# Kernel tuning notes

Measured on AMD Instinct MI355X. Metric: run time of the kernel, lower is better.

Reference implementation:

```python
import jax, jax.numpy as jnp
import numpy as np

EPS = 1e-12  # tf.math.l2_normalize epsilon

def _l2n(x, axis):
    # faithful to K.l2_normalize: x / sqrt(max(sum(x^2), eps))
    return x / jnp.sqrt(jnp.maximum(jnp.sum(x * x, axis=axis, keepdims=True), EPS))

def setup_inputs() -> dict:
    key = jax.random.key(0)
    k1, k2, k3 = jax.random.split(key, 3)
    B, T, D, P = 32, 1024, 256, 20
    inp_a = jax.random.normal(k1, (B, T, D), dtype=jnp.float32)
    inp_b = jax.random.normal(k2, (B, T, D), dtype=jnp.float32)
    # 'uniform' keras initializer -> U(-0.05, 0.05)
    W = jax.random.uniform(k3, (P, D), dtype=jnp.float32, minval=-0.05, maxval=0.05)
    return {"inp_a": inp_a, "inp_b": inp_b, "W": W}

def reference(inp_a, inp_b, W):
    # inp_a, inp_b: (B, T, D); W: (P, D)
    oa = _l2n(inp_a, -1)
    ob = _l2n(inp_b, -1)
    # K.batch_dot(ob, oa, axes=[1,1]) -> (B, D, D), contract over seq
    alpha = jnp.einsum('btd,bte->bde', ob, oa)
    alpha = _l2n(alpha, 1)
    # K.batch_dot(ob, alpha, axes=[2,1]) -> (B, T, D)
    hmean = jnp.einsum('btd,bde->bte', ob, alpha)
    # Per perspective i the original computes the (T,T) batch_dot of
    # l2norm(hmean*W_i) and l2norm(inp_a*W_i), then masks with eye(T) and sums
    # -> the diagonal, i.e. per-token cosine similarity. Since both vectors are
    # scaled by the same W_i, cos = <a*h, W_i^2> / (||a*W_i|| * ||h*W_i||),
    # computed directly in linear cost for all perspectives at once.
    W2 = W * W  # (P, D)
    num = jnp.einsum('btd,pd->btp', inp_a * hmean, W2)
    sa = jnp.einsum('btd,pd->btp', inp_a * inp_a, W2)
    sh = jnp.einsum('btd,pd->btp', hmean * hmean, W2)
    persp = num / (jnp.sqrt(jnp.maximum(sa, EPS)) * jnp.sqrt(jnp.maximum(sh, EPS)))
    return (persp, persp)
```

## Files before the change

### kernel.cpp

```cpp
#include <hip/hip_runtime.h>
#include <math.h>

#define BB 32
#define TT 1024
#define DD 256
#define PP 20
constexpr float EPS = 1e-12f;

typedef __attribute__((ext_vector_type(8))) short bf16x8;
typedef __attribute__((ext_vector_type(4))) float f32x4;

static __device__ __forceinline__ unsigned short f2bf(float f) {
    union { float f; unsigned int u; } c; c.f = f;
    const unsigned int u = c.u;
    return (unsigned short)((u + 0x7FFFu + ((u >> 16) & 1u)) >> 16);
}

__global__ __launch_bounds__(256) void k_prep(const float* __restrict__ in,
                                              unsigned short* __restrict__ outT,
                                              unsigned short* __restrict__ outN) {
    __shared__ unsigned short Tls[DD][66];
    const int b = blockIdx.y;
    const int t0 = blockIdx.x * 64;
    const int wave = threadIdx.x >> 6;
    const int lane = threadIdx.x & 63;
    const float* src = in + (size_t)b * TT * DD;
    for (int pass = 0; pass < 16; ++pass) {
        const int tl = pass * 4 + wave;
        const int t = t0 + tl;
        const float4 v =
            *reinterpret_cast<const float4*>(&src[(size_t)t * DD + lane * 4]);
        float ss = v.x * v.x + v.y * v.y + v.z * v.z + v.w * v.w;
#pragma unroll
        for (int off = 32; off; off >>= 1) ss += __shfl_xor(ss, off);
        const float sc = 1.0f / sqrtf(fmaxf(ss, EPS));
        Tls[lane * 4 + 0][tl] = f2bf(v.x * sc);
        Tls[lane * 4 + 1][tl] = f2bf(v.y * sc);
        Tls[lane * 4 + 2][tl] = f2bf(v.z * sc);
        Tls[lane * 4 + 3][tl] = f2bf(v.w * sc);
        if (outN) {
            ushort4 r;
            r.x = f2bf(v.x); r.y = f2bf(v.y); r.z = f2bf(v.z); r.w = f2bf(v.w);
            *reinterpret_cast<ushort4*>(&outN[((size_t)b * TT + t) * DD + lane * 4]) = r;
        }
    }
    __syncthreads();
    const int d = threadIdx.x;
    unsigned short* dst = outT + ((size_t)b * DD + d) * TT + t0;
#pragma unroll
    for (int k = 0; k < 8; ++k) {
        unsigned short tmp[8];
#pragma unroll
        for (int j = 0; j < 8; ++j) tmp[j] = Tls[d][k * 8 + j];
        *reinterpret_cast<uint4*>(&dst[k * 8]) = *reinterpret_cast<const uint4*>(tmp);
    }
}

template <int M, int N, int K, int KS>
__global__ __launch_bounds__(256) void k_gemm(const unsigned short* __restrict__ A,
                                              const unsigned short* __restrict__ B,
                                              float* __restrict__ C) {
    __shared__ unsigned short As[2][64][40];
    __shared__ unsigned short Bs[2][64][40];
    const int tid = threadIdx.x;
    const int b = blockIdx.y;
    constexpr int NTILES = N / 64;
    constexpr int KSL = K / KS;
    const int m0 = (blockIdx.x / NTILES) * 64;
    const int n0 = (blockIdx.x % NTILES) * 64;
    const int kbeg = blockIdx.z * KSL;
    const unsigned short* pA = A + (size_t)b * M * K + (size_t)m0 * K + kbeg;
    const unsigned short* pB = B + (size_t)b * N * K + (size_t)n0 * K + kbeg;
    const int srow = tid >> 2;
    const int skoff = (tid & 3) * 8;
    const int wave = tid >> 6;
    const int lane = tid & 63;
    const int wm = (wave >> 1) * 32;
    const int wn = (wave & 1) * 32;
    const int fr = lane & 15;
    const int fc = lane >> 4;
    f32x4 acc[2][2] = {};
    uint4 ra, rb;

    ra = *reinterpret_cast<const uint4*>(&pA[(size_t)srow * K + skoff]);
    rb = *reinterpret_cast<const uint4*>(&pB[(size_t)srow * K + skoff]);
    *reinterpret_cast<uint4*>(&As[0][srow][skoff]) = ra;
    *reinterpret_cast<uint4*>(&Bs[0][srow][skoff]) = rb;

    constexpr int NT = KSL / 32;
    for (int t = 0; t < NT; ++t) {
        if (t + 1 < NT) {
            const int k0 = (t + 1) * 32;
            ra = *reinterpret_cast<const uint4*>(&pA[(size_t)srow * K + k0 + skoff]);
            rb = *reinterpret_cast<const uint4*>(&pB[(size_t)srow * K + k0 + skoff]);
        }
        __syncthreads();
        const int cur = t & 1;
        bf16x8 af[2], bfr[2];
#pragma unroll
        for (int i = 0; i < 2; ++i) {
            af[i]  = *reinterpret_cast<const bf16x8*>(&As[cur][wm + i * 16 + fr][fc * 8]);
            bfr[i] = *reinterpret_cast<const bf16x8*>(&Bs[cur][wn + i * 16 + fr][fc * 8]);
        }
#pragma unroll
        for (int i = 0; i < 2; ++i)
#pragma unroll
            for (int j = 0; j < 2; ++j)
                acc[i][j] = __builtin_amdgcn_mfma_f32_16x16x32_bf16(af[i], bfr[j],
                                                                    acc[i][j], 0, 0, 0);
        if (t + 1 < NT) {
            const int nxt = (t + 1) & 1;
            *reinterpret_cast<uint4*>(&As[nxt][srow][skoff]) = ra;
            *reinterpret_cast<uint4*>(&Bs[nxt][srow][skoff]) = rb;
        }
    }
    float* pC = C + (size_t)blockIdx.z * BB * M * N + (size_t)b * M * N;
#pragma unroll
    for (int i = 0; i < 2; ++i)
#pragma unroll
        for (int j = 0; j < 2; ++j) {
            const int rbase = m0 + wm + i * 16 + fc * 4;
            const int col = n0 + wn + j * 16 + fr;
#pragma unroll
            for (int r = 0; r < 4; ++r)
                pC[(size_t)(rbase + r) * N + col] = acc[i][j][r];
        }
}

__global__ __launch_bounds__(256) void k_alphanorm2(const float* __restrict__ p0,
                                                    const float* __restrict__ p1,
                                                    unsigned short* __restrict__ dst) {
    const int wave = threadIdx.x >> 6;
    const int lane = threadIdx.x & 63;
    const size_t row = (size_t)blockIdx.x * 4 + wave;
    float4 v = reinterpret_cast<const float4*>(p0 + row * DD)[lane];
    if (p1) {
        const float4 w = reinterpret_cast<const float4*>(p1 + row * DD)[lane];
        v.x += w.x; v.y += w.y; v.z += w.z; v.w += w.w;
    }
    float s = v.x * v.x + v.y * v.y + v.z * v.z + v.w * v.w;
#pragma unroll
    for (int off = 32; off; off >>= 1) s += __shfl_xor(s, off);
    const float sc = 1.0f / sqrtf(fmaxf(s, EPS));
    ushort4 r;
    r.x = f2bf(v.x * sc); r.y = f2bf(v.y * sc);
    r.z = f2bf(v.z * sc); r.w = f2bf(v.w * sc);
    reinterpret_cast<ushort4*>(dst + row * DD)[lane] = r;
}

__global__ __launch_bounds__(256) void k_persp2(const float* __restrict__ inp_a,
                                                const float* __restrict__ hmean,
                                                const float* __restrict__ W,
                                                float* __restrict__ out) {
    __shared__ uint4 Bpk[8 * 2 * 64];
    const int tid = threadIdx.x;
#pragma unroll
    for (int i = 0; i < 4; ++i) {
        const int ne = tid + i * 256;
        const int kstep = ne >> 7;
        const int j = (ne >> 6) & 1;
        const int ln = ne & 63;
        const int p = j * 16 + (ln & 15);
        const int k0 = kstep * 32 + (ln >> 4) * 8;
        unsigned short w8[8];
        if (p < PP) {
#pragma unroll
            for (int e = 0; e < 8; ++e) {
                const float w = W[p * DD + k0 + e];
                w8[e] = f2bf(w * w);
            }
        } else {
#pragma unroll
            for (int e = 0; e < 8; ++e) w8[e] = 0;
        }
        Bpk[ne] = *reinterpret_cast<const uint4*>(w8);
    }
    __syncthreads();

    const int wave = tid >> 6;
    const int lane = tid & 63;
    const int fr = lane & 15;
    const int fc = lane >> 4;
    const size_t row = (size_t)blockIdx.x * 64 + wave * 16 + fr;
    const float* pa = inp_a + row * DD + fc * 8;
    const float* ph = hmean + row * DD + fc * 8;
    const bf16x8* bp = reinterpret_cast<const bf16x8*>(Bpk);

    f32x4 acc[3][2] = {};
    float4 a0 = *reinterpret_cast<const float4*>(pa);
    float4 a1 = *reinterpret_cast<const float4*>(pa + 4);
    float4 h0 = *reinterpret_cast<const float4*>(ph);
    float4 h1 = *reinterpret_cast<const float4*>(ph + 4);

    for (int t = 0; t < 8; ++t) {
        float4 na0, na1, nh0, nh1;
        if (t < 7) {
            na0 = *reinterpret_cast<const float4*>(pa + (t + 1) * 32);
            na1 = *reinterpret_cast<const float4*>(pa + (t + 1) * 32 + 4);
            nh0 = *reinterpret_cast<const float4*>(ph + (t + 1) * 32);
            nh1 = *reinterpret_cast<const float4*>(ph + (t + 1) * 32 + 4);
        }
        const float av[8] = {a0.x, a0.y, a0.z, a0.w, a1.x, a1.y, a1.z, a1.w};
        const float hv[8] = {h0.x, h0.y, h0.z, h0.w, h1.x, h1.y, h1.z, h1.w};
        unsigned short ah[8], aa[8], hh[8];
#pragma unroll
        for (int e = 0; e < 8; ++e) {
            ah[e] = f2bf(av[e] * hv[e]);
            aa[e] = f2bf(av[e] * av[e]);
            hh[e] = f2bf(hv[e] * hv[e]);
        }
        const bf16x8 pf0 = *reinterpret_cast<const bf16x8*>(ah);
        const bf16x8 pf1 = *reinterpret_cast<const bf16x8*>(aa);
        const bf16x8 pf2 = *reinterpret_cast<const bf16x8*>(hh);
        const bf16x8 bf0 = bp[(t * 2 + 0) * 64 + lane];
        const bf16x8 bf1 = bp[(t * 2 + 1) * 64 + lane];
        acc[0][0] = __builtin_amdgcn_mfma_f32_16x16x32_bf16(pf0, bf0, acc[0][0], 0, 0, 0);
        acc[0][1] = __builtin_amdgcn_mfma_f32_16x16x32_bf16(pf0, bf1, acc[0][1], 0, 0, 0);
        acc[1][0] = __builtin_amdgcn_mfma_f32_16x16x32_bf16(pf1, bf0, acc[1][0], 0, 0, 0);
        acc[1][1] = __builtin_amdgcn_mfma_f32_16x16x32_bf16(pf1, bf1, acc[1][1], 0, 0, 0);
        acc[2][0] = __builtin_amdgcn_mfma_f32_16x16x32_bf16(pf2, bf0, acc[2][0], 0, 0, 0);
        acc[2][1] = __builtin_amdgcn_mfma_f32_16x16x32_bf16(pf2, bf1, acc[2][1], 0, 0, 0);
        a0 = na0; a1 = na1; h0 = nh0; h1 = nh1;
    }

    const size_t rowbase = (size_t)blockIdx.x * 64 + wave * 16 + fc * 4;
#pragma unroll
    for (int j = 0; j < 2; ++j) {
        const int p = j * 16 + fr;
        if (p < PP) {
#pragma unroll
            for (int r = 0; r < 4; ++r) {
                const float num = acc[0][j][r];
                const float sa = sqrtf(fmaxf(acc[1][j][r], EPS));
                const float sh = sqrtf(fmaxf(acc[2][j][r], EPS));
                const float v = num / (sa * sh);
                const size_t o = (rowbase + r) * PP + p;
                out[o] = v;
                out[(size_t)BB * TT * PP + o] = v;
            }
        }
    }
}

extern "C" void kernel_launch(void* const* d_in, const int* in_sizes, int n_in,
                              void* d_out, int out_size, void* d_ws, size_t ws_size,
                              hipStream_t stream) {
    const float* inp_a = (const float*)d_in[0];
    const float* inp_b = (const float*)d_in[1];
    const float* W = (const float*)d_in[2];
    float* out = (float*)d_out;

    const size_t NTD = (size_t)BB * TT * DD;
    const size_t NDD = (size_t)BB * DD * DD;
    unsigned short* oaT = (unsigned short*)d_ws;
    unsigned short* obT = oaT + NTD;
    float* hmean = (float*)d_ws;
    unsigned short* bnat = obT + NTD;
    float* aP0 = (float*)(bnat + NTD);
    const bool SPLIT = ws_size >= (size_t)(NTD * 2 * 3 + NDD * 4 * 2 + NDD * 2);
    float* aP1 = SPLIT ? aP0 + NDD : nullptr;
    unsigned short* aTb = (unsigned short*)(aP0 + (SPLIT ? 2 * NDD : NDD));

    k_prep<<<dim3(TT / 64, BB), 256, 0, stream>>>(inp_a, oaT, nullptr);
    k_prep<<<dim3(TT / 64, BB), 256, 0, stream>>>(inp_b, obT, bnat);
    if (SPLIT)
        k_gemm<DD, DD, TT, 2><<<dim3(16, BB, 2), 256, 0, stream>>>(oaT, obT, aP0);
    else
        k_gemm<DD, DD, TT, 1><<<dim3(16, BB, 1), 256, 0, stream>>>(oaT, obT, aP0);
    k_alphanorm2<<<BB * DD / 4, 256, 0, stream>>>(aP0, aP1, aTb);
    k_gemm<TT, DD, DD, 1><<<dim3(64, BB, 1), 256, 0, stream>>>(bnat, aTb, hmean);
    k_persp2<<<BB * TT / 64, 256, 0, stream>>>(inp_a, hmean, W, out);
}
```

Measured before the change: 184.0 us.

## Replace LDS-tiled GEMM with per-wave register-streamed GEMM and store hmean as bf16

The shared-memory double-buffered 64x64 block GEMM is replaced by a kernel in which each wave independently computes a 32x32 tile. Its MFMA fragments are loaded straight from global memory into registers with two-step prefetch, which drops LDS staging and __syncthreads. The hmean GEMM now writes bf16 output, and the perspective kernel reads and unpacks it, halving that intermediate's traffic. The trade-off is no data reuse across waves, so more global and L2 loads, and extra rounding of hmean to bf16.

```diff
diff --git a/kernel.cpp b/kernel.cpp
--- a/kernel.cpp
+++ b/kernel.cpp
@@ -15,6 +15,8 @@
     const unsigned int u = c.u;
     return (unsigned short)((u + 0x7FFFu + ((u >> 16) & 1u)) >> 16);
 }
+#define BF2LO(u) __uint_as_float((u) << 16)
+#define BF2HI(u) __uint_as_float((u) & 0xffff0000u)
 
 __global__ __launch_bounds__(256) void k_prep(const float* __restrict__ in,
                                               unsigned short* __restrict__ outT,
@@ -56,75 +58,69 @@
     }
 }
 
-template <int M, int N, int K, int KS>
-__global__ __launch_bounds__(256) void k_gemm(const unsigned short* __restrict__ A,
-                                              const unsigned short* __restrict__ B,
-                                              float* __restrict__ C) {
-    __shared__ unsigned short As[2][64][40];
-    __shared__ unsigned short Bs[2][64][40];
-    const int tid = threadIdx.x;
-    const int b = blockIdx.y;
-    constexpr int NTILES = N / 64;
-    constexpr int KSL = K / KS;
-    const int m0 = (blockIdx.x / NTILES) * 64;
-    const int n0 = (blockIdx.x % NTILES) * 64;
-    const int kbeg = blockIdx.z * KSL;
-    const unsigned short* pA = A + (size_t)b * M * K + (size_t)m0 * K + kbeg;
-    const unsigned short* pB = B + (size_t)b * N * K + (size_t)n0 * K + kbeg;
-    const int srow = tid >> 2;
-    const int skoff = (tid & 3) * 8;
-    const int wave = tid >> 6;
-    const int lane = tid & 63;
-    const int wm = (wave >> 1) * 32;
-    const int wn = (wave & 1) * 32;
-    const int fr = lane & 15;
-    const int fc = lane >> 4;
+template <int M, int N, int K, int KS, bool OBF>
+__global__ __launch_bounds__(256) void k_gemm2(const unsigned short* __restrict__ A,
+                                               const unsigned short* __restrict__ B,
+                                               void* __restrict__ Cv) {
+    constexpr int MT = M / 32, NTL = N / 32, KSL = K / KS, NSTEP = KSL / 32;
+    const int job = blockIdx.x * 4 + (threadIdx.x >> 6);
+    const int lane = threadIdx.x & 63;
+    const int nt = job % NTL;
+    int r1 = job / NTL;
+    const int mt = r1 % MT; r1 /= MT;
+    const int ks = r1 % KS;
+    const int b = r1 / KS;
+    const int fr = lane & 15, fc = lane >> 4;
+    const unsigned short* pA = A + ((size_t)b * M + mt * 32 + fr) * K + ks * KSL + fc * 8;
+    const unsigned short* pB = B + ((size_t)b * N + nt * 32 + fr) * K + ks * KSL + fc * 8;
+
+    uint4 ra[2][2], rb[2][2];
     f32x4 acc[2][2] = {};
-    uint4 ra, rb;
-
-    ra = *reinterpret_cast<const uint4*>(&pA[(size_t)srow * K + skoff]);
-    rb = *reinterpret_cast<const uint4*>(&pB[(size_t)srow * K + skoff]);
-    *reinterpret_cast<uint4*>(&As[0][srow][skoff]) = ra;
-    *reinterpret_cast<uint4*>(&Bs[0][srow][skoff]) = rb;
-
-    constexpr int NT = KSL / 32;
-    for (int t = 0; t < NT; ++t) {
-        if (t + 1 < NT) {
-            const int k0 = (t + 1) * 32;
-            ra = *reinterpret_cast<const uint4*>(&pA[(size_t)srow * K + k0 + skoff]);
-            rb = *reinterpret_cast<const uint4*>(&pB[(size_t)srow * K + k0 + skoff]);
-        }
-        __syncthreads();
+
+#define LOADSTEP(buf, t)                                                      \
+    {                                                                         \
+        ra[buf][0] = *reinterpret_cast<const uint4*>(&pA[(t) * 32]);          \
+        ra[buf][1] = *reinterpret_cast<const uint4*>(&pA[16 * K + (t) * 32]); \
+        rb[buf][0] = *reinterpret_cast<const uint4*>(&pB[(t) * 32]);          \
+        rb[buf][1] = *reinterpret_cast<const uint4*>(&pB[16 * K + (t) * 32]); \
+    }
+    LOADSTEP(0, 0)
+    if (NSTEP > 1) LOADSTEP(1, 1)
+#pragma unroll
+    for (int t = 0; t < NSTEP; ++t) {
         const int cur = t & 1;
-        bf16x8 af[2], bfr[2];
-#pragma unroll
-        for (int i = 0; i < 2; ++i) {
-            af[i]  = *reinterpret_cast<const bf16x8*>(&As[cur][wm + i * 16 + fr][fc * 8]);
-            bfr[i] = *reinterpret_cast<const bf16x8*>(&Bs[cur][wn + i * 16 + fr][fc * 8]);
-        }
+        const bf16x8 af0 = *reinterpret_cast<const bf16x8*>(&ra[cur][0]);
+        const bf16x8 af1 = *reinterpret_cast<const bf16x8*>(&ra[cur][1]);
+        const bf16x8 bf0 = *reinterpret_cast<const bf16x8*>(&rb[cur][0]);
+        const bf16x8 bf1 = *reinterpret_cast<const bf16x8*>(&rb[cur][1]);
+        acc[0][0] = __builtin_amdgcn_mfma_f32_16x16x32_bf16(af0, bf0, acc[0][0], 0, 0, 0);
+        acc[0][1] = __builtin_amdgcn_mfma_f32_16x16x32_bf16(af0, bf1, acc[0][1], 0, 0, 0);
+        acc[1][0] = __builtin_amdgcn_mfma_f32_16x16x32_bf16(af1, bf0, acc[1][0], 0, 0, 0);
+        acc[1][1] = __builtin_amdgcn_mfma_f32_16x16x32_bf16(af1, bf1, acc[1][1], 0, 0, 0);
+        if (t + 2 < NSTEP) LOADSTEP(cur, t + 2)
+    }
+#undef LOADSTEP
+    if constexpr (OBF) {
+        unsigned short* C = (unsigned short*)Cv + (size_t)b * M * N;
 #pragma unroll
         for (int i = 0; i < 2; ++i)
 #pragma unroll
             for (int j = 0; j < 2; ++j)
-                acc[i][j] = __builtin_amdgcn_mfma_f32_16x16x32_bf16(af[i], bfr[j],
-                                                                    acc[i][j], 0, 0, 0);
-        if (t + 1 < NT) {
-            const int nxt = (t + 1) & 1;
-            *reinterpret_cast<uint4*>(&As[nxt][srow][skoff]) = ra;
-            *reinterpret_cast<uint4*>(&Bs[nxt][srow][skoff]) = rb;
-        }
-    }
-    float* pC = C + (size_t)blockIdx.z * BB * M * N + (size_t)b * M * N;
-#pragma unroll
-    for (int i = 0; i < 2; ++i)
-#pragma unroll
-        for (int j = 0; j < 2; ++j) {
-            const int rbase = m0 + wm + i * 16 + fc * 4;
-            const int col = n0 + wn + j * 16 + fr;
-#pragma unroll
-            for (int r = 0; r < 4; ++r)
-                pC[(size_t)(rbase + r) * N + col] = acc[i][j][r];
-        }
+#pragma unroll
+                for (int r = 0; r < 4; ++r)
+                    C[(size_t)(mt * 32 + i * 16 + fc * 4 + r) * N + nt * 32 + j * 16 + fr] =
+                        f2bf(acc[i][j][r]);
+    } else {
+        float* C = (float*)Cv + ((size_t)ks * BB + b) * M * N;
+#pragma unroll
+        for (int i = 0; i < 2; ++i)
+#pragma unroll
+            for (int j = 0; j < 2; ++j)
+#pragma unroll
+                for (int r = 0; r < 4; ++r)
+                    C[(size_t)(mt * 32 + i * 16 + fc * 4 + r) * N + nt * 32 + j * 16 + fr] =
+                        acc[i][j][r];
+    }
 }
 
 __global__ __launch_bounds__(256) void k_alphanorm2(const float* __restrict__ p0,
@@ -149,7 +145,7 @@
 }
 
 __global__ __launch_bounds__(256) void k_persp2(const float* __restrict__ inp_a,
-                                                const float* __restrict__ hmean,
+                                                const unsigned short* __restrict__ hmeanb,
                                                 const float* __restrict__ W,
                                                 float* __restrict__ out) {
     __shared__ uint4 Bpk[8 * 2 * 64];
@@ -183,25 +179,26 @@
     const int fc = lane >> 4;
     const size_t row = (size_t)blockIdx.x * 64 + wave * 16 + fr;
     const float* pa = inp_a + row * DD + fc * 8;
-    const float* ph = hmean + row * DD + fc * 8;
+    const unsigned short* ph = hmeanb + row * DD + fc * 8;
     const bf16x8* bp = reinterpret_cast<const bf16x8*>(Bpk);
 
     f32x4 acc[3][2] = {};
     float4 a0 = *reinterpret_cast<const float4*>(pa);
     float4 a1 = *reinterpret_cast<const float4*>(pa + 4);
-    float4 h0 = *reinterpret_cast<const float4*>(ph);
-    float4 h1 = *reinterpret_cast<const float4*>(ph + 4);
-
+    uint4 hq = *reinterpret_cast<const uint4*>(ph);
+
+#pragma unroll
     for (int t = 0; t < 8; ++t) {
-        float4 na0, na1, nh0, nh1;
+        float4 na0, na1;
+        uint4 nhq;
         if (t < 7) {
             na0 = *reinterpret_cast<const float4*>(pa + (t + 1) * 32);
             na1 = *reinterpret_cast<const float4*>(pa + (t + 1) * 32 + 4);
-            nh0 = *reinterpret_cast<const float4*>(ph + (t + 1) * 32);
-            nh1 = *reinterpret_cast<const float4*>(ph + (t + 1) * 32 + 4);
+            nhq = *reinterpret_cast<const uint4*>(ph + (t + 1) * 32);
         }
         const float av[8] = {a0.x, a0.y, a0.z, a0.w, a1.x, a1.y, a1.z, a1.w};
-        const float hv[8] = {h0.x, h0.y, h0.z, h0.w, h1.x, h1.y, h1.z, h1.w};
+        const float hv[8] = {BF2LO(hq.x), BF2HI(hq.x), BF2LO(hq.y), BF2HI(hq.y),
+                             BF2LO(hq.z), BF2HI(hq.z), BF2LO(hq.w), BF2HI(hq.w)};
         unsigned short ah[8], aa[8], hh[8];
 #pragma unroll
         for (int e = 0; e < 8; ++e) {
@@ -220,7 +217,7 @@
         acc[1][1] = __builtin_amdgcn_mfma_f32_16x16x32_bf16(pf1, bf1, acc[1][1], 0, 0, 0);
         acc[2][0] = __builtin_amdgcn_mfma_f32_16x16x32_bf16(pf2, bf0, acc[2][0], 0, 0, 0);
         acc[2][1] = __builtin_amdgcn_mfma_f32_16x16x32_bf16(pf2, bf1, acc[2][1], 0, 0, 0);
-        a0 = na0; a1 = na1; h0 = nh0; h1 = nh1;
+        a0 = na0; a1 = na1; hq = nhq;
     }
 
     const size_t rowbase = (size_t)blockIdx.x * 64 + wave * 16 + fc * 4;
@@ -254,7 +251,7 @@
     const size_t NDD = (size_t)BB * DD * DD;
     unsigned short* oaT = (unsigned short*)d_ws;
     unsigned short* obT = oaT + NTD;
-    float* hmean = (float*)d_ws;
+    unsigned short* hmeanb = oaT;
     unsigned short* bnat = obT + NTD;
     float* aP0 = (float*)(bnat + NTD);
     const bool SPLIT = ws_size >= (size_t)(NTD * 2 * 3 + NDD * 4 * 2 + NDD * 2);
@@ -264,10 +261,13 @@
     k_prep<<<dim3(TT / 64, BB), 256, 0, stream>>>(inp_a, oaT, nullptr);
     k_prep<<<dim3(TT / 64, BB), 256, 0, stream>>>(inp_b, obT, bnat);
     if (SPLIT)
-        k_gemm<DD, DD, TT, 2><<<dim3(16, BB, 2), 256, 0, stream>>>(oaT, obT, aP0);
+        k_gemm2<DD, DD, TT, 2, false>
+            <<<BB * 2 * 8 * 8 / 4, 256, 0, stream>>>(oaT, obT, aP0);
     else
-        k_gemm<DD, DD, TT, 1><<<dim3(16, BB, 1), 256, 0, stream>>>(oaT, obT, aP0);
+        k_gemm2<DD, DD, TT, 1, false>
+            <<<BB * 1 * 8 * 8 / 4, 256, 0, stream>>>(oaT, obT, aP0);
     k_alphanorm2<<<BB * DD / 4, 256, 0, stream>>>(aP0, aP1, aTb);
-    k_gemm<TT, DD, DD, 1><<<dim3(64, BB, 1), 256, 0, stream>>>(bnat, aTb, hmean);
-    k_persp2<<<BB * TT / 64, 256, 0, stream>>>(inp_a, hmean, W, out);
-}
+    k_gemm2<TT, DD, DD, 1, true>
+        <<<BB * 1 * 32 * 8 / 4, 256, 0, stream>>>(bnat, aTb, (void*)hmeanb);
+    k_persp2<<<BB * TT / 64, 256, 0, stream>>>(inp_a, hmeanb, W, out);
+}
```

Measured after the change: 209.4 us. 13.8% more time.

## Store hmean as bf16 and deepen GEMM K-tile to 64

Applied to the files above, without the earlier changes.

The second GEMM now writes hmean as bf16 instead of fp32, and the perspective kernel reads and unpacks it. This halves the write and read traffic for the large (B,T,D) intermediate. Separately, the GEMM K-step grows from 32 to 64 with wider shared-memory tiles, which halves the number of barriers per K sweep at the cost of more LDS per block. The perspective loop is also fully unrolled. hmean now carries bf16 rounding before it is squared, which may affect accuracy.

```diff
diff --git a/kernel.cpp b/kernel.cpp
--- a/kernel.cpp
+++ b/kernel.cpp
@@ -15,6 +15,8 @@
     const unsigned int u = c.u;
     return (unsigned short)((u + 0x7FFFu + ((u >> 16) & 1u)) >> 16);
 }
+#define BF2LO(u) __uint_as_float((u) << 16)
+#define BF2HI(u) __uint_as_float((u) & 0xffff0000u)
 
 __global__ __launch_bounds__(256) void k_prep(const float* __restrict__ in,
                                               unsigned short* __restrict__ outT,
@@ -56,12 +58,12 @@
     }
 }
 
-template <int M, int N, int K, int KS>
+template <int M, int N, int K, int KS, bool OBF>
 __global__ __launch_bounds__(256) void k_gemm(const unsigned short* __restrict__ A,
                                               const unsigned short* __restrict__ B,
-                                              float* __restrict__ C) {
-    __shared__ unsigned short As[2][64][40];
-    __shared__ unsigned short Bs[2][64][40];
+                                              void* __restrict__ Cv) {
+    __shared__ unsigned short As[2][64][72];
+    __shared__ unsigned short Bs[2][64][72];
     const int tid = threadIdx.x;
     const int b = blockIdx.y;
     constexpr int NTILES = N / 64;
@@ -72,7 +74,7 @@
     const unsigned short* pA = A + (size_t)b * M * K + (size_t)m0 * K + kbeg;
     const unsigned short* pB = B + (size_t)b * N * K + (size_t)n0 * K + kbeg;
     const int srow = tid >> 2;
-    const int skoff = (tid & 3) * 8;
+    const int sk = (tid & 3) * 16;
     const int wave = tid >> 6;
     const int lane = tid & 63;
     const int wm = (wave >> 1) * 32;
@@ -80,51 +82,74 @@
     const int fr = lane & 15;
     const int fc = lane >> 4;
     f32x4 acc[2][2] = {};
-    uint4 ra, rb;
-
-    ra = *reinterpret_cast<const uint4*>(&pA[(size_t)srow * K + skoff]);
-    rb = *reinterpret_cast<const uint4*>(&pB[(size_t)srow * K + skoff]);
-    *reinterpret_cast<uint4*>(&As[0][srow][skoff]) = ra;
-    *reinterpret_cast<uint4*>(&Bs[0][srow][skoff]) = rb;
-
-    constexpr int NT = KSL / 32;
+    uint4 ra0, ra1, rb0, rb1;
+
+    ra0 = *reinterpret_cast<const uint4*>(&pA[(size_t)srow * K + sk]);
+    ra1 = *reinterpret_cast<const uint4*>(&pA[(size_t)srow * K + sk + 8]);
+    rb0 = *reinterpret_cast<const uint4*>(&pB[(size_t)srow * K + sk]);
+    rb1 = *reinterpret_cast<const uint4*>(&pB[(size_t)srow * K + sk + 8]);
+    *reinterpret_cast<uint4*>(&As[0][srow][sk]) = ra0;
+    *reinterpret_cast<uint4*>(&As[0][srow][sk + 8]) = ra1;
+    *reinterpret_cast<uint4*>(&Bs[0][srow][sk]) = rb0;
+    *reinterpret_cast<uint4*>(&Bs[0][srow][sk + 8]) = rb1;
+
+    constexpr int NT = KSL / 64;
     for (int t = 0; t < NT; ++t) {
         if (t + 1 < NT) {
-            const int k0 = (t + 1) * 32;
-            ra = *reinterpret_cast<const uint4*>(&pA[(size_t)srow * K + k0 + skoff]);
-            rb = *reinterpret_cast<const uint4*>(&pB[(size_t)srow * K + k0 + skoff]);
+            const int k0 = (t + 1) * 64;
+            ra0 = *reinterpret_cast<const uint4*>(&pA[(size_t)srow * K + k0 + sk]);
+            ra1 = *reinterpret_cast<const uint4*>(&pA[(size_t)srow * K + k0 + sk + 8]);
+            rb0 = *reinterpret_cast<const uint4*>(&pB[(size_t)srow * K + k0 + sk]);
+            rb1 = *reinterpret_cast<const uint4*>(&pB[(size_t)srow * K + k0 + sk + 8]);
         }
         __syncthreads();
         const int cur = t & 1;
-        bf16x8 af[2], bfr[2];
-#pragma unroll
-        for (int i = 0; i < 2; ++i) {
-            af[i]  = *reinterpret_cast<const bf16x8*>(&As[cur][wm + i * 16 + fr][fc * 8]);
-            bfr[i] = *reinterpret_cast<const bf16x8*>(&Bs[cur][wn + i * 16 + fr][fc * 8]);
-        }
-#pragma unroll
-        for (int i = 0; i < 2; ++i)
-#pragma unroll
-            for (int j = 0; j < 2; ++j)
-                acc[i][j] = __builtin_amdgcn_mfma_f32_16x16x32_bf16(af[i], bfr[j],
-                                                                    acc[i][j], 0, 0, 0);
+#pragma unroll
+        for (int kh = 0; kh < 2; ++kh) {
+            bf16x8 af[2], bfr[2];
+#pragma unroll
+            for (int i = 0; i < 2; ++i) {
+                af[i] = *reinterpret_cast<const bf16x8*>(
+                    &As[cur][wm + i * 16 + fr][kh * 32 + fc * 8]);
+                bfr[i] = *reinterpret_cast<const bf16x8*>(
+                    &Bs[cur][wn + i * 16 + fr][kh * 32 + fc * 8]);
+            }
+#pragma unroll
+            for (int i = 0; i < 2; ++i)
+#pragma unroll
+                for (int j = 0; j < 2; ++j)
+                    acc[i][j] = __builtin_amdgcn_mfma_f32_16x16x32_bf16(
+                        af[i], bfr[j], acc[i][j], 0, 0, 0);
+        }
         if (t + 1 < NT) {
             const int nxt = (t + 1) & 1;
-            *reinterpret_cast<uint4*>(&As[nxt][srow][skoff]) = ra;
-            *reinterpret_cast<uint4*>(&Bs[nxt][srow][skoff]) = rb;
-        }
-    }
-    float* pC = C + (size_t)blockIdx.z * BB * M * N + (size_t)b * M * N;
-#pragma unroll
-    for (int i = 0; i < 2; ++i)
-#pragma unroll
-        for (int j = 0; j < 2; ++j) {
-            const int rbase = m0 + wm + i * 16 + fc * 4;
-            const int col = n0 + wn + j * 16 + fr;
-#pragma unroll
-            for (int r = 0; r < 4; ++r)
-                pC[(size_t)(rbase + r) * N + col] = acc[i][j][r];
-        }
+            *reinterpret_cast<uint4*>(&As[nxt][srow][sk]) = ra0;
+            *reinterpret_cast<uint4*>(&As[nxt][srow][sk + 8]) = ra1;
+            *reinterpret_cast<uint4*>(&Bs[nxt][srow][sk]) = rb0;
+            *reinterpret_cast<uint4*>(&Bs[nxt][srow][sk + 8]) = rb1;
+        }
+    }
+    if constexpr (OBF) {
+        unsigned short* C = (unsigned short*)Cv + (size_t)b * M * N;
+#pragma unroll
+        for (int i = 0; i < 2; ++i)
+#pragma unroll
+            for (int j = 0; j < 2; ++j)
+#pragma unroll
+                for (int r = 0; r < 4; ++r)
+                    C[(size_t)(m0 + wm + i * 16 + fc * 4 + r) * N + n0 + wn + j * 16 + fr] =
+                        f2bf(acc[i][j][r]);
+    } else {
+        float* C = (float*)Cv + ((size_t)blockIdx.z * BB + b) * M * N;
+#pragma unroll
+        for (int i = 0; i < 2; ++i)
+#pragma unroll
+            for (int j = 0; j < 2; ++j)
+#pragma unroll
+                for (int r = 0; r < 4; ++r)
+                    C[(size_t)(m0 + wm + i * 16 + fc * 4 + r) * N + n0 + wn + j * 16 + fr] =
+                        acc[i][j][r];
+    }
 }
 
 __global__ __launch_bounds__(256) void k_alphanorm2(const float* __restrict__ p0,
@@ -149,7 +174,7 @@
 }
 
 __global__ __launch_bounds__(256) void k_persp2(const float* __restrict__ inp_a,
-                                                const float* __restrict__ hmean,
+                                                const unsigned short* __restrict__ hmeanb,
                                                 const float* __restrict__ W,
                                                 float* __restrict__ out) {
     __shared__ uint4 Bpk[8 * 2 * 64];
@@ -183,25 +208,26 @@
     const int fc = lane >> 4;
     const size_t row = (size_t)blockIdx.x * 64 + wave * 16 + fr;
     const float* pa = inp_a + row * DD + fc * 8;
-    const float* ph = hmean + row * DD + fc * 8;
+    const unsigned short* ph = hmeanb + row * DD + fc * 8;
     const bf16x8* bp = reinterpret_cast<const bf16x8*>(Bpk);
 
     f32x4 acc[3][2] = {};
     float4 a0 = *reinterpret_cast<const float4*>(pa);
     float4 a1 = *reinterpret_cast<const float4*>(pa + 4);
-    float4 h0 = *reinterpret_cast<const float4*>(ph);
-    float4 h1 = *reinterpret_cast<const float4*>(ph + 4);
-
+    uint4 hq = *reinterpret_cast<const uint4*>(ph);
+
+#pragma unroll
     for (int t = 0; t < 8; ++t) {
-        float4 na0, na1, nh0, nh1;
+        float4 na0, na1;
+        uint4 nhq;
         if (t < 7) {
             na0 = *reinterpret_cast<const float4*>(pa + (t + 1) * 32);
             na1 = *reinterpret_cast<const float4*>(pa + (t + 1) * 32 + 4);
-            nh0 = *reinterpret_cast<const float4*>(ph + (t + 1) * 32);
-            nh1 = *reinterpret_cast<const float4*>(ph + (t + 1) * 32 + 4);
+            nhq = *reinterpret_cast<const uint4*>(ph + (t + 1) * 32);
         }
         const float av[8] = {a0.x, a0.y, a0.z, a0.w, a1.x, a1.y, a1.z, a1.w};
-        const float hv[8] = {h0.x, h0.y, h0.z, h0.w, h1.x, h1.y, h1.z, h1.w};
+        const float hv[8] = {BF2LO(hq.x), BF2HI(hq.x), BF2LO(hq.y), BF2HI(hq.y),
+                             BF2LO(hq.z), BF2HI(hq.z), BF2LO(hq.w), BF2HI(hq.w)};
         unsigned short ah[8], aa[8], hh[8];
 #pragma unroll
         for (int e = 0; e < 8; ++e) {
@@ -220,7 +246,7 @@
         acc[1][1] = __builtin_amdgcn_mfma_f32_16x16x32_bf16(pf1, bf1, acc[1][1], 0, 0, 0);
         acc[2][0] = __builtin_amdgcn_mfma_f32_16x16x32_bf16(pf2, bf0, acc[2][0], 0, 0, 0);
         acc[2][1] = __builtin_amdgcn_mfma_f32_16x16x32_bf16(pf2, bf1, acc[2][1], 0, 0, 0);
-        a0 = na0; a1 = na1; h0 = nh0; h1 = nh1;
+        a0 = na0; a1 = na1; hq = nhq;
     }
 
     const size_t rowbase = (size_t)blockIdx.x * 64 + wave * 16 + fc * 4;
@@ -254,7 +280,7 @@
     const size_t NDD = (size_t)BB * DD * DD;
     unsigned short* oaT = (unsigned short*)d_ws;
     unsigned short* obT = oaT + NTD;
-    float* hmean = (float*)d_ws;
+    unsigned short* hmeanb = oaT;
     unsigned short* bnat = obT + NTD;
     float* aP0 = (float*)(bnat + NTD);
     const bool SPLIT = ws_size >= (size_t)(NTD * 2 * 3 + NDD * 4 * 2 + NDD * 2);
@@ -264,10 +290,13 @@
     k_prep<<<dim3(TT / 64, BB), 256, 0, stream>>>(inp_a, oaT, nullptr);
     k_prep<<<dim3(TT / 64, BB), 256, 0, stream>>>(inp_b, obT, bnat);
     if (SPLIT)
-        k_gemm<DD, DD, TT, 2><<<dim3(16, BB, 2), 256, 0, stream>>>(oaT, obT, aP0);
+        k_gemm<DD, DD, TT, 2, false>
+            <<<dim3(16, BB, 2), 256, 0, stream>>>(oaT, obT, aP0);
     else
-        k_gemm<DD, DD, TT, 1><<<dim3(16, BB, 1), 256, 0, stream>>>(oaT, obT, aP0);
+        k_gemm<DD, DD, TT, 1, false>
+            <<<dim3(16, BB, 1), 256, 0, stream>>>(oaT, obT, aP0);
     k_alphanorm2<<<BB * DD / 4, 256, 0, stream>>>(aP0, aP1, aTb);
-    k_gemm<TT, DD, DD, 1><<<dim3(64, BB, 1), 256, 0, stream>>>(bnat, aTb, hmean);
-    k_persp2<<<BB * TT / 64, 256, 0, stream>>>(inp_a, hmean, W, out);
-}
+    k_gemm<TT, DD, DD, 1, true>
+        <<<dim3(64, BB, 1), 256, 0, stream>>>(bnat, aTb, (void*)hmeanb);
+    k_persp2<<<BB * TT / 64, 256, 0, stream>>>(inp_a, hmeanb, W, out);
+}
```

Measured after the change: 178.0 us. -3.3%, faster.
